# Kernel tuning notes

Measured on AMD Instinct MI355X. Metric: run time of the kernel, lower is better.

## Reference

```python
import jax, jax.numpy as jnp
import numpy as np

N_NODES = 100000
N_EDGES = 1600000
N_GRAPHS = 1000
X_S = 128
HID = 64


def setup_inputs() -> dict:
    key = jax.random.key(0)
    ks = jax.random.split(key, 12)
    x = jax.random.normal(ks[0], (N_NODES, X_S), dtype=jnp.float32)
    edge_index = jax.random.randint(ks[1], (2, N_EDGES), 0, N_NODES, dtype=jnp.int64)
    batch = jnp.sort(jax.random.randint(ks[2], (N_NODES,), 0, N_GRAPHS, dtype=jnp.int64))
    def lin(k, fin, fout):
        s = 1.0 / np.sqrt(fin)
        kw, kb = jax.random.split(k)
        W = jax.random.uniform(kw, (fin, fout), minval=-s, maxval=s, dtype=jnp.float32)
        b = jax.random.uniform(kb, (fout,), minval=-s, maxval=s, dtype=jnp.float32)
        return W, b
    W1, b1 = lin(ks[3], X_S, HID)
    W2, b2 = lin(ks[4], HID, HID)
    W3, b3 = lin(ks[5], HID, HID)
    Wf, bf = lin(ks[6], HID, 10)
    Wl, bl = lin(ks[7], 10, 1)
    eps1 = jnp.float32(0.37)
    eps2 = jnp.float32(0.72)
    eps3 = jnp.float32(0.11)
    return {"x": x, "edge_index": edge_index, "batch": batch,
            "W1": W1, "b1": b1, "W2": W2, "b2": b2, "W3": W3, "b3": b3,
            "Wf": Wf, "bf": bf, "Wl": Wl, "bl": bl,
            "eps1": eps1, "eps2": eps2, "eps3": eps3}


def _gin_conv(h, src, dst, eps, W, b):
    # GIN: nn((1+eps)*x_i + sum_{j in N(i)} x_j); messages flow src -> dst
    agg = jax.ops.segment_sum(h[src], dst, num_segments=N_NODES)  # [N, d]
    return ((1.0 + eps) * h + agg) @ W + b


def reference(x, edge_index, batch, W1, b1, W2, b2, W3, b3, Wf, bf, Wl, bl,
              eps1, eps2, eps3):
    src, dst = edge_index[0], edge_index[1]
    h = jax.nn.relu(_gin_conv(x, src, dst, eps1, W1, b1))
    h = jax.nn.relu(_gin_conv(h, src, dst, eps2, W2, b2))
    h = jax.nn.relu(_gin_conv(h, src, dst, eps3, W3, b3))
    # global_mean_pool over graph ids
    sums = jax.ops.segment_sum(h, batch, num_segments=N_GRAPHS)        # [G, 64]
    cnts = jax.ops.segment_sum(jnp.ones((N_NODES,), h.dtype), batch,
                               num_segments=N_GRAPHS)                   # [G]
    pooled = sums / jnp.maximum(cnts, 1.0)[:, None]
    out = jax.nn.relu(pooled @ Wf + bf) @ Wl + bl                       # [G, 1]
    return out
```

## Files before the change

kernel.cpp:

```cpp
#include <hip/hip_runtime.h>

#define N_NODES 100000
#define N_EDGES 1600000
#define N_GRAPHS 1000

#define NB_C 782
#define B1   256
#define CHUNK (N_EDGES / B1)
#define MTOT (NB_C * B1)

typedef unsigned int uint32;
typedef unsigned short ushort16;
typedef __attribute__((ext_vector_type(8))) short short8;
typedef __attribute__((ext_vector_type(4))) float f32x4;

static __device__ __forceinline__ ushort16 f2bf(float f) {
    uint32 u = __float_as_uint(f);
    u += 0x7fffu + ((u >> 16) & 1u);
    return (ushort16)(u >> 16);
}
static __device__ __forceinline__ uint32 pk2(float a, float b) {
    return (uint32)f2bf(a) | ((uint32)f2bf(b) << 16);
}
static __device__ __forceinline__ void bf2x(uint32 v, float& lo, float& hi) {
    lo = __uint_as_float(v << 16);
    hi = __uint_as_float(v & 0xffff0000u);
}
static __device__ __forceinline__ void acc8(float* a, uint4 v) {
    float lo, hi;
    bf2x(v.x, lo, hi); a[0] += lo; a[1] += hi;
    bf2x(v.y, lo, hi); a[2] += lo; a[3] += hi;
    bf2x(v.z, lo, hi); a[4] += lo; a[5] += hi;
    bf2x(v.w, lo, hi); a[6] += lo; a[7] += hi;
}

union CV8 { uint4 u; short8 s; };

__global__ __launch_bounds__(256) void convw_kernel(
    const float* __restrict__ W1, const float* __restrict__ W2,
    const float* __restrict__ W3,
    ushort16* __restrict__ W1t, ushort16* __restrict__ W2t,
    ushort16* __restrict__ W3t)
{
    int t = threadIdx.x;
    if (blockIdx.x == 0) {
        for (int i = t; i < 64 * 128; i += 256) {
            int j = i >> 7, k = i & 127;
            W1t[i] = f2bf(W1[k * 64 + j]);
        }
    } else if (blockIdx.x == 1) {
        for (int i = t; i < 64 * 64; i += 256) {
            int j = i >> 6, k = i & 63;
            W2t[i] = f2bf(W2[k * 64 + j]);
        }
    } else {
        for (int i = t; i < 64 * 64; i += 256) {
            int j = i >> 6, k = i & 63;
            W3t[i] = f2bf(W3[k * 64 + j]);
        }
    }
}


__global__ __launch_bounds__(256) void count_kernel(
    const int* __restrict__ dst, int* __restrict__ M)
{
    __shared__ int cnt[NB_C];
    int b = blockIdx.x, t = threadIdx.x;
    for (int q = t; q < NB_C; q += 256) cnt[q] = 0;
    __syncthreads();
    int e0 = b * CHUNK;
    for (int e = e0 + t; e < e0 + CHUNK; e += 256)
        atomicAdd(&cnt[dst[e] >> 7], 1);
    __syncthreads();
    for (int q = t; q < NB_C; q += 256) M[q * B1 + b] = cnt[q];
}

#define SCAN_B 1024
#define SCAN_NBLK ((MTOT + SCAN_B - 1) / SCAN_B)

__global__ __launch_bounds__(256) void scanA_kernel(
    const int* __restrict__ in, int* __restrict__ excl, int* __restrict__ bsum)
{
    __shared__ int s[256];
    int b = blockIdx.x, t = threadIdx.x;
    int base = b * SCAN_B + t * 4;
    int v[4];
#pragma unroll
    for (int i = 0; i < 4; ++i) v[i] = (base + i < MTOT) ? in[base + i] : 0;
    int tsum = v[0] + v[1] + v[2] + v[3];
    s[t] = tsum;
    __syncthreads();
    for (int off = 1; off < 256; off <<= 1) {
        int x = (t >= off) ? s[t - off] : 0;
        __syncthreads();
        s[t] += x;
        __syncthreads();
    }
    int run = s[t] - tsum;
#pragma unroll
    for (int i = 0; i < 4; ++i) {
        if (base + i < MTOT) excl[base + i] = run;
        run += v[i];
    }
    if (t == 255) bsum[b] = s[255];
}

__global__ __launch_bounds__(256) void scanB_kernel(int* __restrict__ bsum)
{
    __shared__ int s[256];
    int t = threadIdx.x;
    int v = (t < SCAN_NBLK) ? bsum[t] : 0;
    s[t] = v;
    __syncthreads();
    for (int off = 1; off < 256; off <<= 1) {
        int x = (t >= off) ? s[t - off] : 0;
        __syncthreads();
        s[t] += x;
        __syncthreads();
    }
    if (t < SCAN_NBLK) bsum[t] = s[t] - v;
}

__global__ __launch_bounds__(256) void scanC_kernel(
    const int* __restrict__ excl, const int* __restrict__ bsum,
    int* __restrict__ out)
{
    int b = blockIdx.x, t = threadIdx.x;
    int add = bsum[b];
    int base = b * SCAN_B + t * 4;
#pragma unroll
    for (int i = 0; i < 4; ++i)
        if (base + i < MTOT) out[base + i] = excl[base + i] + add;
}

__global__ __launch_bounds__(256) void scatter_kernel(
    const int* __restrict__ src, const int* __restrict__ dst,
    const int* __restrict__ Ms, uint32* __restrict__ tmp)
{
    __shared__ int cur[NB_C];
    int b = blockIdx.x, t = threadIdx.x;
    for (int q = t; q < NB_C; q += 256) cur[q] = Ms[q * B1 + b];
    __syncthreads();
    int e0 = b * CHUNK;
    for (int e = e0 + t; e < e0 + CHUNK; e += 256) {
        int d = dst[e];
        int q = d >> 7;
        int pos = atomicAdd(&cur[q], 1);
        tmp[pos] = ((uint32)(d & 127) << 17) | (uint32)src[e];
    }
}

__global__ __launch_bounds__(256) void finalize_kernel(
    const uint32* __restrict__ tmp, const int* __restrict__ Ms,
    int* __restrict__ row_off, int* __restrict__ esrc)
{
    __shared__ int cnt[128];
    __shared__ int pref[128];
    __shared__ int cur[128];
    int q = blockIdx.x, t = threadIdx.x;
    int start = Ms[q * B1];
    int end = (q == NB_C - 1) ? N_EDGES : Ms[(q + 1) * B1];

    if (t < 128) cnt[t] = 0;
    __syncthreads();
    for (int e = start + t; e < end; e += 256)
        atomicAdd(&cnt[tmp[e] >> 17], 1);
    __syncthreads();
    if (t < 128) pref[t] = cnt[t];
    __syncthreads();
    for (int off = 1; off < 128; off <<= 1) {
        int x = 0;
        if (t < 128 && t >= off) x = pref[t - off];
        __syncthreads();
        if (t < 128) pref[t] += x;
        __syncthreads();
    }
    if (t < 128) {
        int excl = pref[t] - cnt[t];
        int node = q * 128 + t;
        if (node < N_NODES) row_off[node] = start + excl;
        cur[t] = start + excl;
    }
    if (q == 0 && t == 0) row_off[N_NODES] = N_EDGES;
    __syncthreads();
    for (int e = start + t; e < end; e += 256) {
        uint32 u = tmp[e];
        int pos = atomicAdd(&cur[u >> 17], 1);
        esrc[pos] = (int)(u & 0x1FFFFu);
    }
}

__global__ __launch_bounds__(256) void gemm1_mfma_kernel(
    const float* __restrict__ x,
    const ushort16* __restrict__ Wt,
    ushort16* __restrict__ y)
{
    int lane = threadIdx.x & 63;
    int wave = threadIdx.x >> 6;
    int col = lane & 15, quad = lane >> 4;
    int node0 = blockIdx.x * 64 + wave * 16;
    int anode = node0 + col;

    short8 a[4];
    if (anode < N_NODES) {
        const float* xr = &x[(size_t)anode * 128 + quad * 8];
#pragma unroll
        for (int s = 0; s < 4; ++s) {
            float4 v0 = *(const float4*)&xr[s * 32];
            float4 v1 = *(const float4*)&xr[s * 32 + 4];
            CV8 cv;
            cv.u = make_uint4(pk2(v0.x, v0.y), pk2(v0.z, v0.w),
                              pk2(v1.x, v1.y), pk2(v1.z, v1.w));
            a[s] = cv.s;
        }
    } else {
        short8 z = {0, 0, 0, 0, 0, 0, 0, 0};
#pragma unroll
        for (int s = 0; s < 4; ++s) a[s] = z;
    }

    f32x4 acc[4];
#pragma unroll
    for (int nt = 0; nt < 4; ++nt)
#pragma unroll
        for (int r = 0; r < 4; ++r) acc[nt][r] = 0.0f;

#pragma unroll
    for (int nt = 0; nt < 4; ++nt) {
        const ushort16* wr = &Wt[(size_t)(nt * 16 + col) * 128 + quad * 8];
#pragma unroll
        for (int s = 0; s < 4; ++s) {
            short8 b = *(const short8*)&wr[s * 32];
            acc[nt] = __builtin_amdgcn_mfma_f32_16x16x32_bf16(a[s], b, acc[nt], 0, 0, 0);
        }
    }

#pragma unroll
    for (int nt = 0; nt < 4; ++nt)
#pragma unroll
        for (int r = 0; r < 4; ++r) {
            int node = node0 + quad * 4 + r;
            if (node < N_NODES)
                y[(size_t)node * 64 + nt * 16 + col] = f2bf(acc[nt][r]);
        }
}

__global__ __launch_bounds__(256) void aggregate_kernel(
    const uint4* __restrict__ y4,
    const int* __restrict__ row_off,
    const int* __restrict__ esrc,
    const float* __restrict__ b,
    const float* __restrict__ eps_p,
    uint4* __restrict__ out4)
{
    int lane = threadIdx.x & 63;
    int wave = threadIdx.x >> 6;
    int grp = lane >> 3;
    int w = lane & 7;
    int node = blockIdx.x * 32 + wave * 8 + grp;

    int s0 = row_off[node], s1 = row_off[node + 1];
    float a[8], c[8];
#pragma unroll
    for (int i = 0; i < 8; ++i) { a[i] = 0.f; c[i] = 0.f; }

    int e = s0;
    for (; e + 3 < s1; e += 4) {
        int i0 = esrc[e];
        int i1 = esrc[e + 1];
        int i2 = esrc[e + 2];
        int i3 = esrc[e + 3];
        uint4 v0 = y4[(size_t)i0 * 8 + w];
        uint4 v1 = y4[(size_t)i1 * 8 + w];
        uint4 v2 = y4[(size_t)i2 * 8 + w];
        uint4 v3 = y4[(size_t)i3 * 8 + w];
        acc8(a, v0);
        acc8(c, v1);
        acc8(a, v2);
        acc8(c, v3);
    }
    for (; e < s1; ++e) {
        uint4 v0 = y4[(size_t)esrc[e] * 8 + w];
        acc8(a, v0);
    }
#pragma unroll
    for (int i = 0; i < 8; ++i) a[i] += c[i];

    uint4 sv = y4[(size_t)node * 8 + w];
    float s[8];
    bf2x(sv.x, s[0], s[1]);
    bf2x(sv.y, s[2], s[3]);
    bf2x(sv.z, s[4], s[5]);
    bf2x(sv.w, s[6], s[7]);
    float ep1 = 1.0f + eps_p[0];
    float4 b0 = *(const float4*)&b[w * 8];
    float4 b1 = *(const float4*)&b[w * 8 + 4];
    float r0 = fmaxf(fmaf(ep1, s[0], a[0]) + b0.x, 0.0f);
    float r1 = fmaxf(fmaf(ep1, s[1], a[1]) + b0.y, 0.0f);
    float r2 = fmaxf(fmaf(ep1, s[2], a[2]) + b0.z, 0.0f);
    float r3 = fmaxf(fmaf(ep1, s[3], a[3]) + b0.w, 0.0f);
    float r4 = fmaxf(fmaf(ep1, s[4], a[4]) + b1.x, 0.0f);
    float r5 = fmaxf(fmaf(ep1, s[5], a[5]) + b1.y, 0.0f);
    float r6 = fmaxf(fmaf(ep1, s[6], a[6]) + b1.z, 0.0f);
    float r7 = fmaxf(fmaf(ep1, s[7], a[7]) + b1.w, 0.0f);
    out4[(size_t)node * 8 + w] =
        make_uint4(pk2(r0, r1), pk2(r2, r3), pk2(r4, r5), pk2(r6, r7));
}

__global__ __launch_bounds__(256) void agg_gemm_fused_kernel(
    const uint4* __restrict__ h4,
    const int* __restrict__ row_off,
    const int* __restrict__ esrc,
    const ushort16* __restrict__ Wt,
    const float* __restrict__ bias,
    const float* __restrict__ eps_p,
    ushort16* __restrict__ hout)
{
    __shared__ __align__(16) ushort16 zl[4][16][72];
    int lane = threadIdx.x & 63;
    int wave = threadIdx.x >> 6;
    int g = lane >> 2;
    int c = lane & 3;
    int node0 = blockIdx.x * 64 + wave * 16;
    if (node0 >= N_NODES) return;
    int node = node0 + g;

    int s0 = row_off[node], s1 = row_off[node + 1];
    float a[16], d[16];
#pragma unroll
    for (int i = 0; i < 16; ++i) { a[i] = 0.f; d[i] = 0.f; }

    const size_t cb = (size_t)c * 2;
    int e = s0;
    for (; e + 3 < s1; e += 4) {
        int i0 = esrc[e];
        int i1 = esrc[e + 1];
        int i2 = esrc[e + 2];
        int i3 = esrc[e + 3];
        uint4 v0a = h4[(size_t)i0 * 8 + cb], v0b = h4[(size_t)i0 * 8 + cb + 1];
        uint4 v1a = h4[(size_t)i1 * 8 + cb], v1b = h4[(size_t)i1 * 8 + cb + 1];
        uint4 v2a = h4[(size_t)i2 * 8 + cb], v2b = h4[(size_t)i2 * 8 + cb + 1];
        uint4 v3a = h4[(size_t)i3 * 8 + cb], v3b = h4[(size_t)i3 * 8 + cb + 1];
        acc8(a, v0a); acc8(a + 8, v0b);
        acc8(d, v1a); acc8(d + 8, v1b);
        acc8(a, v2a); acc8(a + 8, v2b);
        acc8(d, v3a); acc8(d + 8, v3b);
    }
    for (; e < s1; ++e) {
        int i0 = esrc[e];
        uint4 va = h4[(size_t)i0 * 8 + cb], vb = h4[(size_t)i0 * 8 + cb + 1];
        acc8(a, va); acc8(a + 8, vb);
    }
#pragma unroll
    for (int i = 0; i < 16; ++i) a[i] += d[i];

    uint4 sva = h4[(size_t)node * 8 + cb], svb = h4[(size_t)node * 8 + cb + 1];
    float s[16];
    bf2x(sva.x, s[0], s[1]);  bf2x(sva.y, s[2], s[3]);
    bf2x(sva.z, s[4], s[5]);  bf2x(sva.w, s[6], s[7]);
    bf2x(svb.x, s[8], s[9]);  bf2x(svb.y, s[10], s[11]);
    bf2x(svb.z, s[12], s[13]); bf2x(svb.w, s[14], s[15]);
    float ep1 = 1.0f + eps_p[0];
    float z[16];
#pragma unroll
    for (int i = 0; i < 16; ++i) z[i] = fmaf(ep1, s[i], a[i]);

    uint4 pA = make_uint4(pk2(z[0], z[1]), pk2(z[2], z[3]),
                          pk2(z[4], z[5]), pk2(z[6], z[7]));
    uint4 pB = make_uint4(pk2(z[8], z[9]), pk2(z[10], z[11]),
                          pk2(z[12], z[13]), pk2(z[14], z[15]));
    *(uint4*)&zl[wave][g][c * 16] = pA;
    *(uint4*)&zl[wave][g][c * 16 + 8] = pB;

    int col = lane & 15, quad = lane >> 4;
    short8 a0 = *(const short8*)&zl[wave][col][quad * 8];
    short8 a1 = *(const short8*)&zl[wave][col][32 + quad * 8];

    f32x4 acc[4];
#pragma unroll
    for (int nt = 0; nt < 4; ++nt)
#pragma unroll
        for (int r = 0; r < 4; ++r) acc[nt][r] = 0.0f;

#pragma unroll
    for (int nt = 0; nt < 4; ++nt) {
        const ushort16* wr = &Wt[(size_t)(nt * 16 + col) * 64 + quad * 8];
        short8 b0 = *(const short8*)&wr[0];
        short8 b1 = *(const short8*)&wr[32];
        acc[nt] = __builtin_amdgcn_mfma_f32_16x16x32_bf16(a0, b0, acc[nt], 0, 0, 0);
        acc[nt] = __builtin_amdgcn_mfma_f32_16x16x32_bf16(a1, b1, acc[nt], 0, 0, 0);
    }

#pragma unroll
    for (int nt = 0; nt < 4; ++nt) {
        float bl = bias[nt * 16 + col];
#pragma unroll
        for (int r = 0; r < 4; ++r) {
            int nd = node0 + quad * 4 + r;
            hout[(size_t)nd * 64 + nt * 16 + col] =
                f2bf(fmaxf(acc[nt][r] + bl, 0.0f));
        }
    }
}

__global__ __launch_bounds__(256) void pool_head_kernel(
    const uint32* __restrict__ hb,
    const int* __restrict__ batch,
    const float* __restrict__ Wf,
    const float* __restrict__ bfv,
    const float* __restrict__ Wl,
    const float* __restrict__ blv,
    float* __restrict__ out)
{
    __shared__ float red[4][64];
    __shared__ float pooled[64];
    __shared__ float hid[10];
    int g = blockIdx.x;
    int t = threadIdx.x;
    int lo = 0, hi = N_NODES;
    while (lo < hi) { int mid = (lo + hi) >> 1; if (batch[mid] < g) lo = mid + 1; else hi = mid; }
    int start = lo;
    hi = N_NODES;
    while (lo < hi) { int mid = (lo + hi) >> 1; if (batch[mid] < g + 1) lo = mid + 1; else hi = mid; }
    int end = lo;

    int c = t & 63, nl = t >> 6;
    int wd = c >> 1, odd = c & 1;
    float acc = 0.0f;
    for (int i = start + nl; i < end; i += 4) {
        uint32 u = hb[(size_t)i * 32 + wd];
        acc += __uint_as_float(odd ? (u & 0xffff0000u) : (u << 16));
    }
    red[nl][c] = acc;
    __syncthreads();
    if (t < 64) {
        float cnt = (float)(end - start);
        float inv = 1.0f / fmaxf(cnt, 1.0f);
        pooled[t] = (red[0][t] + red[1][t] + red[2][t] + red[3][t]) * inv;
    }
    __syncthreads();
    if (t < 10) {
        float s = bfv[t];
#pragma unroll
        for (int k = 0; k < 64; ++k) s = fmaf(pooled[k], Wf[k * 10 + t], s);
        hid[t] = fmaxf(s, 0.0f);
    }
    __syncthreads();
    if (t == 0) {
        float s = blv[0];
#pragma unroll
        for (int j = 0; j < 10; ++j) s = fmaf(hid[j], Wl[j], s);
        out[g] = s;
    }
}

extern "C" void kernel_launch(void* const* d_in, const int* in_sizes, int n_in,
                              void* d_out, int out_size, void* d_ws, size_t ws_size,
                              hipStream_t stream)
{
    const float* x     = (const float*)d_in[0];
    const int*   ei    = (const int*)  d_in[1];
    const int*   src   = ei;
    const int*   dst   = ei + N_EDGES;
    const int*   batch = (const int*)  d_in[2];
    const float* W1    = (const float*)d_in[3];
    const float* b1    = (const float*)d_in[4];
    const float* W2    = (const float*)d_in[5];
    const float* b2    = (const float*)d_in[6];
    const float* W3    = (const float*)d_in[7];
    const float* b3    = (const float*)d_in[8];
    const float* Wf    = (const float*)d_in[9];
    const float* bfv   = (const float*)d_in[10];
    const float* Wl    = (const float*)d_in[11];
    const float* blv   = (const float*)d_in[12];
    const float* eps1  = (const float*)d_in[13];
    const float* eps2  = (const float*)d_in[14];
    const float* eps3  = (const float*)d_in[15];

    ushort16* ybA = (ushort16*)d_ws;
    ushort16* ybB = ybA + (size_t)N_NODES * 64;
    int*   ints = (int*)(ybB + (size_t)N_NODES * 64);
    int*   M       = ints;
    int*   Mex     = M + MTOT;
    int*   Ms      = Mex + MTOT;
    int*   bsum    = Ms + MTOT;
    int*   row_off = bsum + 256;
    int*   esrc    = row_off + N_NODES + 1;
    uint32* tmp    = (uint32*)(esrc + N_EDGES);
    ushort16* W1t = (ushort16*)(((uintptr_t)(tmp + N_EDGES) + 255) & ~(uintptr_t)255);
    ushort16* W2t = W1t + 64 * 128;
    ushort16* W3t = W2t + 64 * 64;

    const int gemm_blk  = (N_NODES + 63) / 64;
    const int agg_blk   = N_NODES / 32;
    const int fused_blk = (N_NODES + 63) / 64;

    convw_kernel<<<3, 256, 0, stream>>>(W1, W2, W3, W1t, W2t, W3t);

    count_kernel<<<B1, 256, 0, stream>>>(dst, M);
    scanA_kernel<<<SCAN_NBLK, 256, 0, stream>>>(M, Mex, bsum);
    scanB_kernel<<<1, 256, 0, stream>>>(bsum);
    scanC_kernel<<<SCAN_NBLK, 256, 0, stream>>>(Mex, bsum, Ms);
    scatter_kernel<<<B1, 256, 0, stream>>>(src, dst, Ms, tmp);
    finalize_kernel<<<NB_C, 256, 0, stream>>>(tmp, Ms, row_off, esrc);

    gemm1_mfma_kernel<<<gemm_blk, 256, 0, stream>>>(x, W1t, ybA);
    aggregate_kernel<<<agg_blk, 256, 0, stream>>>(
        (const uint4*)ybA, row_off, esrc, b1, eps1, (uint4*)ybB);

    agg_gemm_fused_kernel<<<fused_blk, 256, 0, stream>>>(
        (const uint4*)ybB, row_off, esrc, W2t, b2, eps2, ybA);

    agg_gemm_fused_kernel<<<fused_blk, 256, 0, stream>>>(
        (const uint4*)ybA, row_off, esrc, W3t, b3, eps3, ybB);

    pool_head_kernel<<<N_GRAPHS, 256, 0, stream>>>(
        (const uint32*)ybB, batch, Wf, bfv, Wl, blv, (float*)d_out);
}
```

Before: 312.3 us.

## Stage per-block edge scatter in LDS and widen buckets to 256 nodes

```diff
diff --git a/kernel.cpp b/kernel.cpp
--- a/kernel.cpp
+++ b/kernel.cpp
@@ -4,7 +4,7 @@
 #define N_EDGES 1600000
 #define N_GRAPHS 1000
 
-#define NB_C 782
+#define NB_C 391
 #define B1   256
 #define CHUNK (N_EDGES / B1)
 #define MTOT (NB_C * B1)
@@ -71,7 +71,7 @@
     __syncthreads();
     int e0 = b * CHUNK;
     for (int e = e0 + t; e < e0 + CHUNK; e += 256)
-        atomicAdd(&cnt[dst[e] >> 7], 1);
+        atomicAdd(&cnt[dst[e] >> 8], 1);
     __syncthreads();
     for (int q = t; q < NB_C; q += 256) M[q * B1 + b] = cnt[q];
 }
@@ -138,16 +138,41 @@
     const int* __restrict__ src, const int* __restrict__ dst,
     const int* __restrict__ Ms, uint32* __restrict__ tmp)
 {
+    __shared__ int cnt[NB_C];
+    __shared__ int loc[NB_C + 1];
     __shared__ int cur[NB_C];
+    __shared__ uint32 staged[CHUNK];
     int b = blockIdx.x, t = threadIdx.x;
-    for (int q = t; q < NB_C; q += 256) cur[q] = Ms[q * B1 + b];
-    __syncthreads();
     int e0 = b * CHUNK;
+
+    for (int q = t; q < NB_C; q += 256) cnt[q] = 0;
+    __syncthreads();
+    for (int e = e0 + t; e < e0 + CHUNK; e += 256)
+        atomicAdd(&cnt[dst[e] >> 8], 1);
+    __syncthreads();
+    if (t == 0) {
+        int r = 0;
+        for (int q = 0; q < NB_C; ++q) { loc[q] = r; r += cnt[q]; }
+        loc[NB_C] = r;
+    }
+    __syncthreads();
+    for (int q = t; q < NB_C; q += 256) cur[q] = loc[q];
+    __syncthreads();
     for (int e = e0 + t; e < e0 + CHUNK; e += 256) {
         int d = dst[e];
-        int q = d >> 7;
+        int q = d >> 8;
         int pos = atomicAdd(&cur[q], 1);
-        tmp[pos] = ((uint32)(d & 127) << 17) | (uint32)src[e];
+        staged[pos] = ((uint32)(d & 255) << 17) | (uint32)src[e];
+    }
+    __syncthreads();
+    for (int i = t; i < CHUNK; i += 256) {
+        int lo = 0, hi = NB_C - 1;
+        while (lo < hi) {
+            int mid = (lo + hi + 1) >> 1;
+            if (loc[mid] <= i) lo = mid; else hi = mid - 1;
+        }
+        int gpos = Ms[lo * B1 + b] + (i - loc[lo]);
+        tmp[gpos] = staged[i];
     }
 }
 
@@ -155,30 +180,29 @@
     const uint32* __restrict__ tmp, const int* __restrict__ Ms,
     int* __restrict__ row_off, int* __restrict__ esrc)
 {
-    __shared__ int cnt[128];
-    __shared__ int pref[128];
-    __shared__ int cur[128];
+    __shared__ int cnt[256];
+    __shared__ int pref[256];
+    __shared__ int cur[256];
     int q = blockIdx.x, t = threadIdx.x;
     int start = Ms[q * B1];
     int end = (q == NB_C - 1) ? N_EDGES : Ms[(q + 1) * B1];
 
-    if (t < 128) cnt[t] = 0;
+    cnt[t] = 0;
     __syncthreads();
     for (int e = start + t; e < end; e += 256)
         atomicAdd(&cnt[tmp[e] >> 17], 1);
     __syncthreads();
-    if (t < 128) pref[t] = cnt[t];
-    __syncthreads();
-    for (int off = 1; off < 128; off <<= 1) {
-        int x = 0;
-        if (t < 128 && t >= off) x = pref[t - off];
+    pref[t] = cnt[t];
+    __syncthreads();
+    for (int off = 1; off < 256; off <<= 1) {
+        int x = (t >= off) ? pref[t - off] : 0;
         __syncthreads();
-        if (t < 128) pref[t] += x;
+        pref[t] += x;
         __syncthreads();
     }
-    if (t < 128) {
+    {
         int excl = pref[t] - cnt[t];
-        int node = q * 128 + t;
+        int node = q * 256 + t;
         if (node < N_NODES) row_off[node] = start + excl;
         cur[t] = start + excl;
     }
```

Measured after the change: 333.4 us. 1.07x slower.
